# Kernel optimization log

Measured on AMD Instinct MI355X. Metric: run time of the kernel, lower is better.

The kernel has to match this reference:

```python
import jax, jax.numpy as jnp
import numpy as np
from jax import lax

B, S, N, FD = 4, 12, 307, 3
E = 64; F = 64; H = 64; K = 3; HEADS = 4; P = 12; DFF = 64


def setup_inputs() -> dict:
    key = jax.random.key(0)
    ks = jax.random.split(key, 24)
    rn = lambda i, shape, s=0.1: jax.random.normal(ks[i], shape, dtype=jnp.float32) * s
    z = lambda n: jnp.zeros((n,), jnp.float32)
    return {
        'x': jax.random.normal(ks[0], (B, S, N, FD), dtype=jnp.float32),
        'cheb': rn(1, (K, N, N), 0.05),
        'theta': rn(2, (K, E, F)),
        'W_emb_x': rn(3, (1, E)), 'b_emb_x': z(E),
        'W_emb_os': rn(4, (FD - 1, E)), 'b_emb_os': z(E),
        'U_x': rn(5, (F, 4 * H)), 'V_x': rn(6, (H, 4 * H)), 'b_x': z(4 * H),
        'U_g': rn(7, (F, 2 * H)), 'V_g': rn(8, (H, 2 * H)), 'b_g': z(2 * H),
        'W_ff1': rn(9, (H, DFF)), 'b_ff1': z(DFF), 'W_ff2': rn(10, (DFF, H)), 'b_ff2': z(H),
        'W_tc': rn(11, (F, H, 1, 3)), 'b_tc': z(F),
        'W_rc': rn(12, (F, H, 1, 1)), 'b_rc': z(F),
        'W_in': rn(13, (3 * F, F)), 'b_in': z(3 * F),
        'W_out': rn(14, (F, F)), 'b_out': z(F),
        'W_fa1': rn(15, (F, DFF)), 'b_fa1': z(DFF), 'W_fa2': rn(16, (DFF, F)), 'b_fa2': z(F),
        'W_fin': rn(17, (P, S, 1, F)), 'b_fin': z(P),
    }


def _forward(x, cheb, theta, W_emb_x, b_emb_x, W_emb_os, b_emb_os,
             U_x, V_x, b_x, U_g, V_g, b_g, W_ff1, b_ff1, W_ff2, b_ff2,
             W_tc, b_tc, W_rc, b_rc, W_in, b_in, W_out, b_out,
             W_fa1, b_fa1, W_fa2, b_fa2, W_fin, b_fin):
    # token embeddings (dropout=0 -> identity)
    emb_x = x[..., :1] @ W_emb_x + b_emb_x          # (B,S,N,E)
    emb_os = x[..., 1:] @ W_emb_os + b_emb_os       # (B,S,N,E)

    def cheb_conv(h):
        # sum_k relu-after-sum of T_k @ h @ theta_k
        agg = jnp.einsum('kmn,bsnc->kbsmc', cheb, h)
        return jax.nn.relu(jnp.einsum('kbsmc,kcd->bsmd', agg, theta))

    gcn_x = cheb_conv(emb_x)                        # (B,S,N,F)
    gcn_os = cheb_conv(emb_os)                      # (B,S,N,F)

    # Glstm: precompute input projections, scan the recurrence over time
    gx = jnp.einsum('bsnc,cf->sbnf', gcn_x, U_x) + b_x    # (S,B,N,4H)
    gg = jnp.einsum('bsnc,cf->sbnf', gcn_os, U_g) + b_g   # (S,B,N,2H)

    h0 = jnp.zeros((B, N, H), x.dtype)
    c0 = jnp.zeros((B, N, H), x.dtype)

    def step(carry, inp):
        ht, ct = carry
        gx_t, gg_t = inp
        gates = jax.nn.sigmoid(gx_t + ht @ V_x)     # ft,it,ot,ut all sigmoid (as in source)
        gov = jax.nn.sigmoid(gg_t + ht @ V_g)
        ft, it, ot, ut = jnp.split(gates, 4, axis=-1)
        gf, gu = jnp.split(gov, 2, axis=-1)
        ct = gf * ft * ct + gu * it * ut
        ht = ot * jnp.tanh(ct)
        return (ht, ct), ht

    _, hs = lax.scan(step, (h0, c0), (gx, gg))
    hidden = jnp.moveaxis(hs, 0, 1)                 # (B,S,N,H)
    # Muti_glstm output feedforward
    hidden = jax.nn.relu(hidden @ W_ff1 + b_ff1) @ W_ff2 + b_ff2

    # time conv: (1,3) kernel over time axis, pad 1
    hs_nchw = jnp.transpose(hidden, (0, 3, 2, 1))   # (B,H,N,S)
    tc = lax.conv_general_dilated(hs_nchw, W_tc, (1, 1), ((0, 0), (1, 1)),
                                  dimension_numbers=('NCHW', 'OIHW', 'NCHW'))
    tc = jnp.transpose(tc + b_tc[None, :, None, None], (0, 3, 2, 1))  # (B,S,N,F)

    # query = last time step, repeated over S
    query = jnp.broadcast_to(tc[:, -1:], (B, S, N, F))
    q_in = jnp.reshape(jnp.swapaxes(query, 2, 3), (B * N, S, F))
    kv_in = jnp.reshape(jnp.swapaxes(emb_x, 2, 3), (B * N, S, E))

    # torch MHA (batch_first=False): seq axis is dim0 (L=B*N), batch axis is dim1 (S)
    hd = F // HEADS
    Wq, Wk, Wv = jnp.split(W_in, 3, axis=0)
    bq, bk, bv = jnp.split(b_in, 3)

    def proj(t, Wp, bp):
        L = t.shape[0]
        p = t @ Wp.T + bp                            # (L, S, F)
        return jnp.transpose(p.reshape(L, S * HEADS, hd), (1, 0, 2))  # (S*HEADS, L, hd)

    qh = proj(q_in, Wq, bq)
    kh = proj(kv_in, Wk, bk)
    vh = proj(kv_in, Wv, bv)
    scores = jnp.einsum('hld,hmd->hlm', qh, kh) / np.float32(np.sqrt(hd))
    attn = jax.nn.softmax(scores, axis=-1)
    ctx = jnp.einsum('hlm,hmd->hld', attn, vh)       # (S*HEADS, B*N, hd)
    ctx = jnp.transpose(ctx, (1, 0, 2)).reshape(B * N, S, F)
    dsa = ctx @ W_out.T + b_out                      # (B*N, S, F)

    dsa = jnp.swapaxes(dsa.reshape(B, N, S, F), 1, 2)  # (B,S,N,F)
    ffa = jax.nn.relu(dsa @ W_fa1 + b_fa1) @ W_fa2 + b_fa2
    # residual 1x1 conv over channels of hidden
    res = jnp.einsum('bsnh,fh->bsnf', hidden, W_rc[:, :, 0, 0]) + b_rc
    comb = res + ffa                                 # (B,S,N,F)
    # final conv: channels=S, kernel (1,F) valid, then take last width index
    out = jnp.einsum('bsnf,psf->bpn', comb, W_fin[:, :, 0, :]) + b_fin[None, :, None]
    return out                                       # (B, pre_len, N)


def reference(x, cheb, theta, W_emb_x, b_emb_x, W_emb_os, b_emb_os,
              U_x, V_x, b_x, U_g, V_g, b_g, W_ff1, b_ff1, W_ff2, b_ff2,
              W_tc, b_tc, W_rc, b_rc, W_in, b_in, W_out, b_out,
              W_fa1, b_fa1, W_fa2, b_fa2, W_fin, b_fin):
    return _forward(x, cheb, theta, W_emb_x, b_emb_x, W_emb_os, b_emb_os,
                    U_x, V_x, b_x, U_g, V_g, b_g, W_ff1, b_ff1, W_ff2, b_ff2,
                    W_tc, b_tc, W_rc, b_rc, W_in, b_in, W_out, b_out,
                    W_fa1, b_fa1, W_fa2, b_fa2, W_fin, b_fin)
```

## Files before the change

kernel.cpp:

```cpp
#include <hip/hip_runtime.h>
#include <hip/hip_bf16.h>

#define BB 4
#define SS 12
#define NN 307
#define LL 1228
#define BSC 48
#define GG 48
#define WS_CX    0
#define WS_CROW  132624
#define WS_TXD   133568
#define WS_TBD   133760
#define WS_T1D   133952
#define WS_T2D   134144
#define WS_TOB   134336
#define WS_WRCT  134528
#define WS_WOT   138624
#define WS_H2    142720
#define WS_TFL   1085824
#define WS_XFL   1164416
#define WS_QH    2107520
#define WS_KH    3050624
#define WS_VH    3993728
#define WS_CTX   4936832

__global__ __launch_bounds__(256) void k1_precomp(
    const float* __restrict__ theta, const float* __restrict__ Wex,
    const float* __restrict__ bex, const float* __restrict__ Weos,
    const float* __restrict__ beos, const float* __restrict__ W_rc,
    const float* __restrict__ W_out, float* __restrict__ ws) {
  int tid = threadIdx.x;
  if (tid < 192) {
    int k = tid / 64, d = tid % 64;
    float a0 = 0.f, a1 = 0.f, a2 = 0.f, a3 = 0.f, a4 = 0.f;
    for (int c = 0; c < 64; ++c) {
      float th = theta[(k * 64 + c) * 64 + d];
      a0 = fmaf(Wex[c], th, a0);
      a1 = fmaf(bex[c], th, a1);
      a2 = fmaf(Weos[c], th, a2);
      a3 = fmaf(Weos[64 + c], th, a3);
      a4 = fmaf(beos[c], th, a4);
    }
    ws[WS_TXD + tid] = a0; ws[WS_TBD + tid] = a1; ws[WS_T1D + tid] = a2;
    ws[WS_T2D + tid] = a3; ws[WS_TOB + tid] = a4;
  }
  for (int i = tid; i < 4096; i += 256) {
    int hh = i >> 6, f = i & 63;
    ws[WS_WRCT + i] = W_rc[f * 64 + hh];
    ws[WS_WOT + i]  = W_out[f * 64 + hh];
  }
}

__global__ __launch_bounds__(320) void k2_cx(const float* __restrict__ x,
                                             const float* __restrict__ cheb,
                                             float* __restrict__ ws) {
  int k = blockIdx.x / BSC, bs = blockIdx.x % BSC;
  __shared__ float xl[921];
  for (int i = threadIdx.x; i < 921; i += 320) xl[i] = x[bs * 921 + i];
  __syncthreads();
  int m = threadIdx.x;
  if (m < NN) {
    const float* ch = cheb + (k * NN + m) * NN;
    float a0 = 0.f, a1 = 0.f, a2 = 0.f, ar = 0.f;
    for (int n = 0; n < NN; ++n) {
      float c = ch[n];
      ar += c;
      a0 = fmaf(c, xl[3 * n], a0);
      a1 = fmaf(c, xl[3 * n + 1], a1);
      a2 = fmaf(c, xl[3 * n + 2], a2);
    }
    ws[WS_CX + ((k * 3 + 0) * BSC + bs) * NN + m] = a0;
    ws[WS_CX + ((k * 3 + 1) * BSC + bs) * NN + m] = a1;
    ws[WS_CX + ((k * 3 + 2) * BSC + bs) * NN + m] = a2;
    if (bs == 0) ws[WS_CROW + k * NN + m] = ar;
  }
}

__global__ __launch_bounds__(256) void k2c_xfl(const float* __restrict__ x,
                                               const float* __restrict__ Wex,
                                               const float* __restrict__ bex,
                                               float* __restrict__ ws) {
  int idx = blockIdx.x * 256 + threadIdx.x;
  if (idx < 943104) {
    int n = idx % NN;
    int t = idx / NN;
    int e = t & 63;
    int bs = t >> 6;
    ws[WS_XFL + idx] = fmaf(x[(bs * NN + n) * 3], Wex[e], bex[e]);
  }
}

__global__ __launch_bounds__(384) void k3_scan(
    const float* __restrict__ U_x, const float* __restrict__ V_x,
    const float* __restrict__ b_x, const float* __restrict__ U_g,
    const float* __restrict__ V_g, const float* __restrict__ b_g,
    const float* __restrict__ W_ff1, const float* __restrict__ b_ff1,
    const float* __restrict__ W_ff2, const float* __restrict__ b_ff2,
    const float* __restrict__ W_tc, const float* __restrict__ b_tc,
    float* __restrict__ ws) {
  int l = blockIdx.x;
  int b = l / NN, n = l % NN;
  int tid = threadIdx.x;
  __shared__ float gcx[768], gcos[768], hsb[768], sg[256], sv[128];

  for (int idx = tid; idx < 768; idx += 384) {
    int s = idx >> 6, d = idx & 63;
    int bs = b * SS + s;
    float ax = 0.f, ao = 0.f;
#pragma unroll
    for (int k = 0; k < 3; ++k) {
      float c0 = ws[WS_CX + ((k * 3 + 0) * BSC + bs) * NN + n];
      float c1 = ws[WS_CX + ((k * 3 + 1) * BSC + bs) * NN + n];
      float c2 = ws[WS_CX + ((k * 3 + 2) * BSC + bs) * NN + n];
      float cr = ws[WS_CROW + k * NN + n];
      ax += c0 * ws[WS_TXD + k * 64 + d] + cr * ws[WS_TBD + k * 64 + d];
      ao += c1 * ws[WS_T1D + k * 64 + d] + c2 * ws[WS_T2D + k * 64 + d] +
            cr * ws[WS_TOB + k * 64 + d];
    }
    gcx[idx] = fmaxf(ax, 0.f);
    gcos[idx] = fmaxf(ao, 0.f);
  }
  __syncthreads();

  float gr[12];
  float vcol[64];
  if (tid < 256) {
#pragma unroll
    for (int s = 0; s < 12; ++s) gr[s] = b_x[tid];
    for (int c4 = 0; c4 < 16; ++c4) {
      float u0 = U_x[(4 * c4 + 0) * 256 + tid];
      float u1 = U_x[(4 * c4 + 1) * 256 + tid];
      float u2 = U_x[(4 * c4 + 2) * 256 + tid];
      float u3 = U_x[(4 * c4 + 3) * 256 + tid];
#pragma unroll
      for (int s = 0; s < 12; ++s) {
        float4 g = *reinterpret_cast<const float4*>(&gcx[s * 64 + 4 * c4]);
        gr[s] = fmaf(g.x, u0, fmaf(g.y, u1, fmaf(g.z, u2, fmaf(g.w, u3, gr[s]))));
      }
    }
#pragma unroll
    for (int c = 0; c < 64; ++c) vcol[c] = V_x[c * 256 + tid];
  } else {
    int j = tid - 256;
#pragma unroll
    for (int s = 0; s < 12; ++s) gr[s] = b_g[j];
    for (int c4 = 0; c4 < 16; ++c4) {
      float u0 = U_g[(4 * c4 + 0) * 128 + j];
      float u1 = U_g[(4 * c4 + 1) * 128 + j];
      float u2 = U_g[(4 * c4 + 2) * 128 + j];
      float u3 = U_g[(4 * c4 + 3) * 128 + j];
#pragma unroll
      for (int s = 0; s < 12; ++s) {
        float4 g = *reinterpret_cast<const float4*>(&gcos[s * 64 + 4 * c4]);
        gr[s] = fmaf(g.x, u0, fmaf(g.y, u1, fmaf(g.z, u2, fmaf(g.w, u3, gr[s]))));
      }
    }
#pragma unroll
    for (int c = 0; c < 64; ++c) vcol[c] = V_g[c * 128 + j];
  }

  float ct = 0.f;
  for (int s = 0; s < 12; ++s) {
    float a = gr[s];
    if (s > 0) {
      const float* hp = &hsb[(s - 1) * 64];
      float a0 = 0.f, a1 = 0.f, a2 = 0.f, a3 = 0.f;
#pragma unroll
      for (int c4 = 0; c4 < 16; c4 += 4) {
        float4 h0 = *reinterpret_cast<const float4*>(&hp[4 * c4]);
        float4 h1 = *reinterpret_cast<const float4*>(&hp[4 * c4 + 4]);
        float4 h2 = *reinterpret_cast<const float4*>(&hp[4 * c4 + 8]);
        float4 h3 = *reinterpret_cast<const float4*>(&hp[4 * c4 + 12]);
        a0 = fmaf(h0.x, vcol[4 * c4 + 0], fmaf(h0.y, vcol[4 * c4 + 1],
             fmaf(h0.z, vcol[4 * c4 + 2], fmaf(h0.w, vcol[4 * c4 + 3], a0))));
        a1 = fmaf(h1.x, vcol[4 * c4 + 4], fmaf(h1.y, vcol[4 * c4 + 5],
             fmaf(h1.z, vcol[4 * c4 + 6], fmaf(h1.w, vcol[4 * c4 + 7], a1))));
        a2 = fmaf(h2.x, vcol[4 * c4 + 8], fmaf(h2.y, vcol[4 * c4 + 9],
             fmaf(h2.z, vcol[4 * c4 + 10], fmaf(h2.w, vcol[4 * c4 + 11], a2))));
        a3 = fmaf(h3.x, vcol[4 * c4 + 12], fmaf(h3.y, vcol[4 * c4 + 13],
             fmaf(h3.z, vcol[4 * c4 + 14], fmaf(h3.w, vcol[4 * c4 + 15], a3))));
      }
      a += (a0 + a1) + (a2 + a3);
    }
    float sig = 1.f / (1.f + __expf(-a));
    if (tid < 256) sg[tid] = sig; else sv[tid - 256] = sig;
    __syncthreads();
    if (tid < 64) {
      ct = sv[tid] * sg[tid] * ct + sv[64 + tid] * sg[64 + tid] * sg[192 + tid];
      hsb[s * 64 + tid] = sg[128 + tid] * tanhf(ct);
    }
    __syncthreads();
  }

  for (int idx = tid; idx < 768; idx += 384) {
    int s = idx >> 6, d = idx & 63;
    float acc = b_ff1[d];
    for (int c4 = 0; c4 < 16; ++c4) {
      float4 h4 = *reinterpret_cast<const float4*>(&hsb[s * 64 + 4 * c4]);
      acc = fmaf(h4.x, W_ff1[(4 * c4 + 0) * 64 + d],
            fmaf(h4.y, W_ff1[(4 * c4 + 1) * 64 + d],
            fmaf(h4.z, W_ff1[(4 * c4 + 2) * 64 + d],
            fmaf(h4.w, W_ff1[(4 * c4 + 3) * 64 + d], acc))));
    }
    gcx[idx] = fmaxf(acc, 0.f);
  }
  __syncthreads();
  for (int idx = tid; idx < 768; idx += 384) {
    int s = idx >> 6, h = idx & 63;
    float acc = b_ff2[h];
    for (int c4 = 0; c4 < 16; ++c4) {
      float4 t4 = *reinterpret_cast<const float4*>(&gcx[s * 64 + 4 * c4]);
      acc = fmaf(t4.x, W_ff2[(4 * c4 + 0) * 64 + h],
            fmaf(t4.y, W_ff2[(4 * c4 + 1) * 64 + h],
            fmaf(t4.z, W_ff2[(4 * c4 + 2) * 64 + h],
            fmaf(t4.w, W_ff2[(4 * c4 + 3) * 64 + h], acc))));
    }
    ws[WS_H2 + ((b * SS + s) * NN + n) * 64 + h] = acc;
    gcos[idx] = acc;
  }
  __syncthreads();
  if (tid < 64) {
    int f = tid;
    float acc = b_tc[f];
    for (int h = 0; h < 64; ++h) {
      acc = fmaf(gcos[10 * 64 + h], W_tc[(f * 64 + h) * 3 + 0], acc);
      acc = fmaf(gcos[11 * 64 + h], W_tc[(f * 64 + h) * 3 + 1], acc);
    }
    ws[WS_TFL + (b * 64 + f) * NN + n] = acc;
  }
}

__global__ __launch_bounds__(256) void k5_qkv(const float* __restrict__ W_in,
                                              const float* __restrict__ b_in,
                                              float* __restrict__ ws) {
  int blk = blockIdx.x;
  int g = blk / 77, mt = blk % 77;
  int s = g >> 2, a = g & 3;
  int m0 = mt * 16;
  __shared__ float xw[16][64], qw[16][64];
  for (int i = threadIdx.x; i < 1024; i += 256) {
    int mi = i >> 6, e = i & 63;
    int m = m0 + mi;
    if (m < LL) {
      int base = m * 768 + s * 64;
      xw[mi][e] = ws[WS_XFL + base + e];
      int bq = base / 235776;
      int off = base % 19648;
      qw[mi][e] = ws[WS_TFL + bq * 19648 + off + e];
    }
  }
  __syncthreads();
  int mi = threadIdx.x >> 4, d = threadIdx.x & 15;
  int m = m0 + mi;
  if (m < LL) {
    int f = a * 16 + d;
    float aq = b_in[f], ak = b_in[64 + f], av = b_in[128 + f];
    for (int e = 0; e < 64; ++e) {
      aq = fmaf(qw[mi][e], W_in[f * 64 + e], aq);
      ak = fmaf(xw[mi][e], W_in[(64 + f) * 64 + e], ak);
      av = fmaf(xw[mi][e], W_in[(128 + f) * 64 + e], av);
    }
    int o = (g * LL + m) * 16 + d;
    ws[WS_QH + o] = aq; ws[WS_KH + o] = ak; ws[WS_VH + o] = av;
  }
}

__global__ __launch_bounds__(512) void k6_attn(float* __restrict__ ws) {
  int blk = blockIdx.x;
  int g = blk / 10, qt = blk % 10;
  int s = g >> 2, a = g & 3;
  int tid = threadIdx.x;
  int w = tid >> 6;
  int qi = tid & 63;
  int l0 = qt * 128 + qi;
  int l1 = l0 + 64;
  bool act0 = (l0 < LL), act1 = (l1 < LL);

  __shared__ float sh[9728];
  float4* kt4 = reinterpret_cast<float4*>(sh);
  float4* vt4 = reinterpret_cast<float4*>(sh + 4096);

  float q0[16], q1[16], cx0[16], cx1[16];
  if (act0) {
    const float4* qp = reinterpret_cast<const float4*>(ws + WS_QH + (g * LL + l0) * 16);
#pragma unroll
    for (int jj = 0; jj < 4; ++jj) {
      float4 t = qp[jj];
      q0[4 * jj] = t.x * 0.25f; q0[4 * jj + 1] = t.y * 0.25f;
      q0[4 * jj + 2] = t.z * 0.25f; q0[4 * jj + 3] = t.w * 0.25f;
    }
  } else {
#pragma unroll
    for (int d = 0; d < 16; ++d) q0[d] = 0.f;
  }
  if (act1) {
    const float4* qp = reinterpret_cast<const float4*>(ws + WS_QH + (g * LL + l1) * 16);
#pragma unroll
    for (int jj = 0; jj < 4; ++jj) {
      float4 t = qp[jj];
      q1[4 * jj] = t.x * 0.25f; q1[4 * jj + 1] = t.y * 0.25f;
      q1[4 * jj + 2] = t.z * 0.25f; q1[4 * jj + 3] = t.w * 0.25f;
    }
  } else {
#pragma unroll
    for (int d = 0; d < 16; ++d) q1[d] = 0.f;
  }
#pragma unroll
  for (int d = 0; d < 16; ++d) { cx0[d] = 0.f; cx1[d] = 0.f; }
  float den0 = 0.f, den1 = 0.f;

  const float4* kb = reinterpret_cast<const float4*>(ws + WS_KH + g * LL * 16);
  const float4* vb = reinterpret_cast<const float4*>(ws + WS_VH + g * LL * 16);

  for (int mt = 0; mt < 5; ++mt) {
    int mbase = mt * 256;
    int cnt = LL - mbase; if (cnt > 256) cnt = 256;
    int nf4 = cnt * 4;
    for (int i = tid; i < nf4; i += 512) {
      kt4[i] = kb[mbase * 4 + i];
      vt4[i] = vb[mbase * 4 + i];
    }
    __syncthreads();
    int e0 = w * 32;
    int e1 = e0 + 32; if (e1 > cnt) e1 = cnt;
    for (int mi = e0; mi < e1; ++mi) {
      float4 ka = kt4[mi * 4], kbb = kt4[mi * 4 + 1];
      float4 kc = kt4[mi * 4 + 2], kd = kt4[mi * 4 + 3];
      float p0 = q0[0] * ka.x, p1 = q1[0] * ka.x;
      p0 = fmaf(q0[1], ka.y, p0);   p1 = fmaf(q1[1], ka.y, p1);
      p0 = fmaf(q0[2], ka.z, p0);   p1 = fmaf(q1[2], ka.z, p1);
      p0 = fmaf(q0[3], ka.w, p0);   p1 = fmaf(q1[3], ka.w, p1);
      p0 = fmaf(q0[4], kbb.x, p0);  p1 = fmaf(q1[4], kbb.x, p1);
      p0 = fmaf(q0[5], kbb.y, p0);  p1 = fmaf(q1[5], kbb.y, p1);
      p0 = fmaf(q0[6], kbb.z, p0);  p1 = fmaf(q1[6], kbb.z, p1);
      p0 = fmaf(q0[7], kbb.w, p0);  p1 = fmaf(q1[7], kbb.w, p1);
      p0 = fmaf(q0[8], kc.x, p0);   p1 = fmaf(q1[8], kc.x, p1);
      p0 = fmaf(q0[9], kc.y, p0);   p1 = fmaf(q1[9], kc.y, p1);
      p0 = fmaf(q0[10], kc.z, p0);  p1 = fmaf(q1[10], kc.z, p1);
      p0 = fmaf(q0[11], kc.w, p0);  p1 = fmaf(q1[11], kc.w, p1);
      p0 = fmaf(q0[12], kd.x, p0);  p1 = fmaf(q1[12], kd.x, p1);
      p0 = fmaf(q0[13], kd.y, p0);  p1 = fmaf(q1[13], kd.y, p1);
      p0 = fmaf(q0[14], kd.z, p0);  p1 = fmaf(q1[14], kd.z, p1);
      p0 = fmaf(q0[15], kd.w, p0);  p1 = fmaf(q1[15], kd.w, p1);
      float e0w = __expf(fminf(p0, 60.f));
      float e1w = __expf(fminf(p1, 60.f));
      den0 += e0w; den1 += e1w;
      float4 va = vt4[mi * 4], vbb = vt4[mi * 4 + 1];
      float4 vc = vt4[mi * 4 + 2], vd = vt4[mi * 4 + 3];
      cx0[0]  = fmaf(e0w, va.x, cx0[0]);   cx1[0]  = fmaf(e1w, va.x, cx1[0]);
      cx0[1]  = fmaf(e0w, va.y, cx0[1]);   cx1[1]  = fmaf(e1w, va.y, cx1[1]);
      cx0[2]  = fmaf(e0w, va.z, cx0[2]);   cx1[2]  = fmaf(e1w, va.z, cx1[2]);
      cx0[3]  = fmaf(e0w, va.w, cx0[3]);   cx1[3]  = fmaf(e1w, va.w, cx1[3]);
      cx0[4]  = fmaf(e0w, vbb.x, cx0[4]);  cx1[4]  = fmaf(e1w, vbb.x, cx1[4]);
      cx0[5]  = fmaf(e0w, vbb.y, cx0[5]);  cx1[5]  = fmaf(e1w, vbb.y, cx1[5]);
      cx0[6]  = fmaf(e0w, vbb.z, cx0[6]);  cx1[6]  = fmaf(e1w, vbb.z, cx1[6]);
      cx0[7]  = fmaf(e0w, vbb.w, cx0[7]);  cx1[7]  = fmaf(e1w, vbb.w, cx1[7]);
      cx0[8]  = fmaf(e0w, vc.x, cx0[8]);   cx1[8]  = fmaf(e1w, vc.x, cx1[8]);
      cx0[9]  = fmaf(e0w, vc.y, cx0[9]);   cx1[9]  = fmaf(e1w, vc.y, cx1[9]);
      cx0[10] = fmaf(e0w, vc.z, cx0[10]);  cx1[10] = fmaf(e1w, vc.z, cx1[10]);
      cx0[11] = fmaf(e0w, vc.w, cx0[11]);  cx1[11] = fmaf(e1w, vc.w, cx1[11]);
      cx0[12] = fmaf(e0w, vd.x, cx0[12]);  cx1[12] = fmaf(e1w, vd.x, cx1[12]);
      cx0[13] = fmaf(e0w, vd.y, cx0[13]);  cx1[13] = fmaf(e1w, vd.y, cx1[13]);
      cx0[14] = fmaf(e0w, vd.z, cx0[14]);  cx1[14] = fmaf(e1w, vd.z, cx1[14]);
      cx0[15] = fmaf(e0w, vd.w, cx0[15]);  cx1[15] = fmaf(e1w, vd.w, cx1[15]);
    }
    __syncthreads();
  }

  float* sden = sh;
  float* scx  = sh + 512;
#pragma unroll
  for (int ph = 0; ph < 2; ++ph) {
    sden[w * 64 + qi] = ph ? den1 : den0;
    const float* cxp = ph ? cx1 : cx0;
#pragma unroll
    for (int d = 0; d < 16; ++d) scx[(w * 64 + qi) * 17 + d] = cxp[d];
    __syncthreads();
    if (tid < 256) {
      int q2 = tid >> 2, jj = tid & 3;
      int l2 = qt * 128 + ph * 64 + q2;
      if (l2 < LL) {
        float dtot = 0.f, c0 = 0.f, c1 = 0.f, c2 = 0.f, c3 = 0.f;
#pragma unroll
        for (int u = 0; u < 8; ++u) {
          dtot += sden[u * 64 + q2];
          const float* cp = &scx[(u * 64 + q2) * 17 + jj * 4];
          c0 += cp[0]; c1 += cp[1]; c2 += cp[2]; c3 += cp[3];
        }
        float inv = 1.f / dtot;
        float* op = ws + WS_CTX + (l2 * SS + s) * 64 + a * 16 + jj * 4;
        *reinterpret_cast<float4*>(op) =
            make_float4(c0 * inv, c1 * inv, c2 * inv, c3 * inv);
      }
    }
    __syncthreads();
  }
}

__global__ __launch_bounds__(64) void k7a_comb(
    const float* __restrict__ W_fa1, const float* __restrict__ b_fa1,
    const float* __restrict__ W_fa2, const float* __restrict__ b_fa2,
    const float* __restrict__ b_rc, const float* __restrict__ b_out,
    float* __restrict__ ws) {
  int blk = blockIdx.x;
  int l = blk / SS, s = blk % SS;
  int b = l / NN, n = l % NN;
  int f = threadIdx.x;
  __shared__ float h2r[64], ctr[64], dsrL[64], trL[64];

  h2r[f] = ws[WS_H2 + ((b * SS + s) * NN + n) * 64 + f];
  ctr[f] = ws[WS_CTX + (l * SS + s) * 64 + f];
  __syncthreads();

  float dsr = b_out[f], res = b_rc[f];
  for (int q = 0; q < 64; ++q) {
    dsr = fmaf(ctr[q], ws[WS_WOT + q * 64 + f], dsr);
    res = fmaf(h2r[q], ws[WS_WRCT + q * 64 + f], res);
  }
  dsrL[f] = dsr;
  __syncthreads();

  float t = b_fa1[f];
  for (int q = 0; q < 64; ++q) t = fmaf(dsrL[q], W_fa1[q * 64 + f], t);
  trL[f] = fmaxf(t, 0.f);
  __syncthreads();

  float ff = b_fa2[f];
  for (int q = 0; q < 64; ++q) ff = fmaf(trL[q], W_fa2[q * 64 + f], ff);
  ws[WS_XFL + (l * SS + s) * 64 + f] = res + ff;
}

__global__ __launch_bounds__(320) void k7b_fin(
    const float* __restrict__ W_fin, const float* __restrict__ b_fin,
    const float* __restrict__ ws, float* __restrict__ out) {
  int blk = blockIdx.x;
  int b = blk / SS, p = blk % SS;
  int tid = threadIdx.x;
  __shared__ float wf[768];
  for (int i = tid; i < 768; i += 320) wf[i] = W_fin[p * 768 + i];
  __syncthreads();
  int n = tid;
  if (n < NN) {
    const float* cb = ws + WS_XFL + (b * NN + n) * 768;
    float a0 = 0.f, a1 = 0.f, a2 = 0.f, a3 = 0.f;
    for (int i = 0; i < 768; i += 4) {
      a0 = fmaf(cb[i], wf[i], a0);
      a1 = fmaf(cb[i + 1], wf[i + 1], a1);
      a2 = fmaf(cb[i + 2], wf[i + 2], a2);
      a3 = fmaf(cb[i + 3], wf[i + 3], a3);
    }
    out[(b * SS + p) * NN + n] = (a0 + a1) + (a2 + a3) + b_fin[p];
  }
}

extern "C" void kernel_launch(void* const* d_in, const int* in_sizes, int n_in,
                              void* d_out, int out_size, void* d_ws, size_t ws_size,
                              hipStream_t stream) {
  (void)in_sizes; (void)n_in; (void)out_size; (void)ws_size;
  const float* x     = (const float*)d_in[0];
  const float* cheb  = (const float*)d_in[1];
  const float* theta = (const float*)d_in[2];
  const float* Wex   = (const float*)d_in[3];
  const float* bex   = (const float*)d_in[4];
  const float* Weos  = (const float*)d_in[5];
  const float* beos  = (const float*)d_in[6];
  const float* U_x   = (const float*)d_in[7];
  const float* V_x   = (const float*)d_in[8];
  const float* b_x   = (const float*)d_in[9];
  const float* U_g   = (const float*)d_in[10];
  const float* V_g   = (const float*)d_in[11];
  const float* b_g   = (const float*)d_in[12];
  const float* W_ff1 = (const float*)d_in[13];
  const float* b_ff1 = (const float*)d_in[14];
  const float* W_ff2 = (const float*)d_in[15];
  const float* b_ff2 = (const float*)d_in[16];
  const float* W_tc  = (const float*)d_in[17];
  const float* b_tc  = (const float*)d_in[18];
  const float* W_rc  = (const float*)d_in[19];
  const float* b_rc  = (const float*)d_in[20];
  const float* W_in  = (const float*)d_in[21];
  const float* b_in  = (const float*)d_in[22];
  const float* W_out = (const float*)d_in[23];
  const float* b_out = (const float*)d_in[24];
  const float* W_fa1 = (const float*)d_in[25];
  const float* b_fa1 = (const float*)d_in[26];
  const float* W_fa2 = (const float*)d_in[27];
  const float* b_fa2 = (const float*)d_in[28];
  const float* W_fin = (const float*)d_in[29];
  const float* b_fin = (const float*)d_in[30];
  float* ws = (float*)d_ws;
  float* outp = (float*)d_out;

  k1_precomp<<<1, 256, 0, stream>>>(theta, Wex, bex, Weos, beos, W_rc, W_out, ws);
  k2_cx<<<144, 320, 0, stream>>>(x, cheb, ws);
  k2c_xfl<<<3684, 256, 0, stream>>>(x, Wex, bex, ws);
  k3_scan<<<1228, 384, 0, stream>>>(U_x, V_x, b_x, U_g, V_g, b_g,
                                    W_ff1, b_ff1, W_ff2, b_ff2, W_tc, b_tc, ws);
  k5_qkv<<<48 * 77, 256, 0, stream>>>(W_in, b_in, ws);
  k6_attn<<<480, 512, 0, stream>>>(ws);
  k7a_comb<<<LL * SS, 64, 0, stream>>>(W_fa1, b_fa1, W_fa2, b_fa2,
                                       b_rc, b_out, ws);
  k7b_fin<<<BB * SS, 320, 0, stream>>>(W_fin, b_fin, ws, outp);
}
```

Before: 366.1 us.

## Fuse prep kernels and use wave shuffles in LSTM scan to drop a barrier

Merges the three preprocessing kernels into a single launch with block-index dispatch, cutting launch overhead. In the recurrent scan, every wave now redundantly computes the cell state and broadcasts h via wave shuffles instead of LDS. The gate buffers are double-buffered so only one __syncthreads per step is needed. This trades redundant tanh/ALU work and shuffle traffic for fewer barriers and less LDS use.

```diff
diff --git a/kernel.cpp b/kernel.cpp
--- a/kernel.cpp
+++ b/kernel.cpp
@@ -24,69 +24,64 @@
 #define WS_VH    3993728
 #define WS_CTX   4936832
 
-__global__ __launch_bounds__(256) void k1_precomp(
+__global__ __launch_bounds__(320) void k12_fused(
+    const float* __restrict__ x, const float* __restrict__ cheb,
     const float* __restrict__ theta, const float* __restrict__ Wex,
     const float* __restrict__ bex, const float* __restrict__ Weos,
     const float* __restrict__ beos, const float* __restrict__ W_rc,
     const float* __restrict__ W_out, float* __restrict__ ws) {
+  int blk = blockIdx.x;
   int tid = threadIdx.x;
-  if (tid < 192) {
-    int k = tid / 64, d = tid % 64;
-    float a0 = 0.f, a1 = 0.f, a2 = 0.f, a3 = 0.f, a4 = 0.f;
-    for (int c = 0; c < 64; ++c) {
-      float th = theta[(k * 64 + c) * 64 + d];
-      a0 = fmaf(Wex[c], th, a0);
-      a1 = fmaf(bex[c], th, a1);
-      a2 = fmaf(Weos[c], th, a2);
-      a3 = fmaf(Weos[64 + c], th, a3);
-      a4 = fmaf(beos[c], th, a4);
-    }
-    ws[WS_TXD + tid] = a0; ws[WS_TBD + tid] = a1; ws[WS_T1D + tid] = a2;
-    ws[WS_T2D + tid] = a3; ws[WS_TOB + tid] = a4;
-  }
-  for (int i = tid; i < 4096; i += 256) {
-    int hh = i >> 6, f = i & 63;
-    ws[WS_WRCT + i] = W_rc[f * 64 + hh];
-    ws[WS_WOT + i]  = W_out[f * 64 + hh];
-  }
-}
-
-__global__ __launch_bounds__(320) void k2_cx(const float* __restrict__ x,
-                                             const float* __restrict__ cheb,
-                                             float* __restrict__ ws) {
-  int k = blockIdx.x / BSC, bs = blockIdx.x % BSC;
-  __shared__ float xl[921];
-  for (int i = threadIdx.x; i < 921; i += 320) xl[i] = x[bs * 921 + i];
-  __syncthreads();
-  int m = threadIdx.x;
-  if (m < NN) {
-    const float* ch = cheb + (k * NN + m) * NN;
-    float a0 = 0.f, a1 = 0.f, a2 = 0.f, ar = 0.f;
-    for (int n = 0; n < NN; ++n) {
-      float c = ch[n];
-      ar += c;
-      a0 = fmaf(c, xl[3 * n], a0);
-      a1 = fmaf(c, xl[3 * n + 1], a1);
-      a2 = fmaf(c, xl[3 * n + 2], a2);
-    }
-    ws[WS_CX + ((k * 3 + 0) * BSC + bs) * NN + m] = a0;
-    ws[WS_CX + ((k * 3 + 1) * BSC + bs) * NN + m] = a1;
-    ws[WS_CX + ((k * 3 + 2) * BSC + bs) * NN + m] = a2;
-    if (bs == 0) ws[WS_CROW + k * NN + m] = ar;
-  }
-}
-
-__global__ __launch_bounds__(256) void k2c_xfl(const float* __restrict__ x,
-                                               const float* __restrict__ Wex,
-                                               const float* __restrict__ bex,
-                                               float* __restrict__ ws) {
-  int idx = blockIdx.x * 256 + threadIdx.x;
-  if (idx < 943104) {
-    int n = idx % NN;
-    int t = idx / NN;
-    int e = t & 63;
-    int bs = t >> 6;
-    ws[WS_XFL + idx] = fmaf(x[(bs * NN + n) * 3], Wex[e], bex[e]);
+  if (blk < 144) {
+    int k = blk / BSC, bs = blk % BSC;
+    __shared__ float xl[921];
+    for (int i = tid; i < 921; i += 320) xl[i] = x[bs * 921 + i];
+    __syncthreads();
+    int m = tid;
+    if (m < NN) {
+      const float* ch = cheb + (k * NN + m) * NN;
+      float a0 = 0.f, a1 = 0.f, a2 = 0.f, ar = 0.f;
+      for (int n = 0; n < NN; ++n) {
+        float c = ch[n];
+        ar += c;
+        a0 = fmaf(c, xl[3 * n], a0);
+        a1 = fmaf(c, xl[3 * n + 1], a1);
+        a2 = fmaf(c, xl[3 * n + 2], a2);
+      }
+      ws[WS_CX + ((k * 3 + 0) * BSC + bs) * NN + m] = a0;
+      ws[WS_CX + ((k * 3 + 1) * BSC + bs) * NN + m] = a1;
+      ws[WS_CX + ((k * 3 + 2) * BSC + bs) * NN + m] = a2;
+      if (bs == 0) ws[WS_CROW + k * NN + m] = ar;
+    }
+  } else if (blk < 3092) {
+    int idx = (blk - 144) * 320 + tid;
+    if (idx < 943104) {
+      int n = idx % NN;
+      int t = idx / NN;
+      int e = t & 63;
+      int bs = t >> 6;
+      ws[WS_XFL + idx] = fmaf(x[(bs * NN + n) * 3], Wex[e], bex[e]);
+    }
+  } else {
+    if (tid < 192) {
+      int k = tid / 64, d = tid % 64;
+      float a0 = 0.f, a1 = 0.f, a2 = 0.f, a3 = 0.f, a4 = 0.f;
+      for (int c = 0; c < 64; ++c) {
+        float th = theta[(k * 64 + c) * 64 + d];
+        a0 = fmaf(Wex[c], th, a0);
+        a1 = fmaf(bex[c], th, a1);
+        a2 = fmaf(Weos[c], th, a2);
+        a3 = fmaf(Weos[64 + c], th, a3);
+        a4 = fmaf(beos[c], th, a4);
+      }
+      ws[WS_TXD + tid] = a0; ws[WS_TBD + tid] = a1; ws[WS_T1D + tid] = a2;
+      ws[WS_T2D + tid] = a3; ws[WS_TOB + tid] = a4;
+    }
+    for (int i = tid; i < 4096; i += 320) {
+      int hh = i >> 6, f = i & 63;
+      ws[WS_WRCT + i] = W_rc[f * 64 + hh];
+      ws[WS_WOT + i]  = W_out[f * 64 + hh];
+    }
   }
 }
 
@@ -101,7 +96,7 @@
   int l = blockIdx.x;
   int b = l / NN, n = l % NN;
   int tid = threadIdx.x;
-  __shared__ float gcx[768], gcos[768], hsb[768], sg[256], sv[128];
+  __shared__ float gcx[768], gcos[768], hsb[768], sg[512], sv[256];
 
   for (int idx = tid; idx < 768; idx += 384) {
     int s = idx >> 6, d = idx & 63;
@@ -141,14 +136,14 @@
 #pragma unroll
     for (int c = 0; c < 64; ++c) vcol[c] = V_x[c * 256 + tid];
   } else {
-    int j = tid - 256;
-#pragma unroll
-    for (int s = 0; s < 12; ++s) gr[s] = b_g[j];
+    int j2 = tid - 256;
+#pragma unroll
+    for (int s = 0; s < 12; ++s) gr[s] = b_g[j2];
     for (int c4 = 0; c4 < 16; ++c4) {
-      float u0 = U_g[(4 * c4 + 0) * 128 + j];
-      float u1 = U_g[(4 * c4 + 1) * 128 + j];
-      float u2 = U_g[(4 * c4 + 2) * 128 + j];
-      float u3 = U_g[(4 * c4 + 3) * 128 + j];
+      float u0 = U_g[(4 * c4 + 0) * 128 + j2];
+      float u1 = U_g[(4 * c4 + 1) * 128 + j2];
+      float u2 = U_g[(4 * c4 + 2) * 128 + j2];
+      float u3 = U_g[(4 * c4 + 3) * 128 + j2];
 #pragma unroll
       for (int s = 0; s < 12; ++s) {
         float4 g = *reinterpret_cast<const float4*>(&gcos[s * 64 + 4 * c4]);
@@ -156,41 +151,37 @@
       }
     }
 #pragma unroll
-    for (int c = 0; c < 64; ++c) vcol[c] = V_g[c * 128 + j];
-  }
-
-  float ct = 0.f;
+    for (int c = 0; c < 64; ++c) vcol[c] = V_g[c * 128 + j2];
+  }
+
+  int j = tid & 63;
+  float ct = 0.f, h = 0.f;
   for (int s = 0; s < 12; ++s) {
     float a = gr[s];
     if (s > 0) {
-      const float* hp = &hsb[(s - 1) * 64];
       float a0 = 0.f, a1 = 0.f, a2 = 0.f, a3 = 0.f;
 #pragma unroll
-      for (int c4 = 0; c4 < 16; c4 += 4) {
-        float4 h0 = *reinterpret_cast<const float4*>(&hp[4 * c4]);
-        float4 h1 = *reinterpret_cast<const float4*>(&hp[4 * c4 + 4]);
-        float4 h2 = *reinterpret_cast<const float4*>(&hp[4 * c4 + 8]);
-        float4 h3 = *reinterpret_cast<const float4*>(&hp[4 * c4 + 12]);
-        a0 = fmaf(h0.x, vcol[4 * c4 + 0], fmaf(h0.y, vcol[4 * c4 + 1],
-             fmaf(h0.z, vcol[4 * c4 + 2], fmaf(h0.w, vcol[4 * c4 + 3], a0))));
-        a1 = fmaf(h1.x, vcol[4 * c4 + 4], fmaf(h1.y, vcol[4 * c4 + 5],
-             fmaf(h1.z, vcol[4 * c4 + 6], fmaf(h1.w, vcol[4 * c4 + 7], a1))));
-        a2 = fmaf(h2.x, vcol[4 * c4 + 8], fmaf(h2.y, vcol[4 * c4 + 9],
-             fmaf(h2.z, vcol[4 * c4 + 10], fmaf(h2.w, vcol[4 * c4 + 11], a2))));
-        a3 = fmaf(h3.x, vcol[4 * c4 + 12], fmaf(h3.y, vcol[4 * c4 + 13],
-             fmaf(h3.z, vcol[4 * c4 + 14], fmaf(h3.w, vcol[4 * c4 + 15], a3))));
+      for (int c = 0; c < 64; c += 4) {
+        a0 = fmaf(__shfl(h, c + 0, 64), vcol[c + 0], a0);
+        a1 = fmaf(__shfl(h, c + 1, 64), vcol[c + 1], a1);
+        a2 = fmaf(__shfl(h, c + 2, 64), vcol[c + 2], a2);
+        a3 = fmaf(__shfl(h, c + 3, 64), vcol[c + 3], a3);
       }
       a += (a0 + a1) + (a2 + a3);
     }
     float sig = 1.f / (1.f + __expf(-a));
-    if (tid < 256) sg[tid] = sig; else sv[tid - 256] = sig;
-    __syncthreads();
-    if (tid < 64) {
-      ct = sv[tid] * sg[tid] * ct + sv[64 + tid] * sg[64 + tid] * sg[192 + tid];
-      hsb[s * 64 + tid] = sg[128 + tid] * tanhf(ct);
-    }
-    __syncthreads();
-  }
+    int p = s & 1;
+    if (tid < 256) sg[p * 256 + tid] = sig;
+    else sv[p * 128 + (tid - 256)] = sig;
+    __syncthreads();
+    float ft = sg[p * 256 + j],       it = sg[p * 256 + 64 + j];
+    float ot = sg[p * 256 + 128 + j], ut = sg[p * 256 + 192 + j];
+    float gf = sv[p * 128 + j],       gu = sv[p * 128 + 64 + j];
+    ct = gf * ft * ct + gu * it * ut;
+    h = ot * tanhf(ct);
+    if (tid < 64) hsb[s * 64 + j] = h;
+  }
+  __syncthreads();
 
   for (int idx = tid; idx < 768; idx += 384) {
     int s = idx >> 6, d = idx & 63;
@@ -206,25 +197,25 @@
   }
   __syncthreads();
   for (int idx = tid; idx < 768; idx += 384) {
-    int s = idx >> 6, h = idx & 63;
-    float acc = b_ff2[h];
+    int s = idx >> 6, hh = idx & 63;
+    float acc = b_ff2[hh];
     for (int c4 = 0; c4 < 16; ++c4) {
       float4 t4 = *reinterpret_cast<const float4*>(&gcx[s * 64 + 4 * c4]);
-      acc = fmaf(t4.x, W_ff2[(4 * c4 + 0) * 64 + h],
-            fmaf(t4.y, W_ff2[(4 * c4 + 1) * 64 + h],
-            fmaf(t4.z, W_ff2[(4 * c4 + 2) * 64 + h],
-            fmaf(t4.w, W_ff2[(4 * c4 + 3) * 64 + h], acc))));
-    }
-    ws[WS_H2 + ((b * SS + s) * NN + n) * 64 + h] = acc;
+      acc = fmaf(t4.x, W_ff2[(4 * c4 + 0) * 64 + hh],
+            fmaf(t4.y, W_ff2[(4 * c4 + 1) * 64 + hh],
+            fmaf(t4.z, W_ff2[(4 * c4 + 2) * 64 + hh],
+            fmaf(t4.w, W_ff2[(4 * c4 + 3) * 64 + hh], acc))));
+    }
+    ws[WS_H2 + ((b * SS + s) * NN + n) * 64 + hh] = acc;
     gcos[idx] = acc;
   }
   __syncthreads();
   if (tid < 64) {
     int f = tid;
     float acc = b_tc[f];
-    for (int h = 0; h < 64; ++h) {
-      acc = fmaf(gcos[10 * 64 + h], W_tc[(f * 64 + h) * 3 + 0], acc);
-      acc = fmaf(gcos[11 * 64 + h], W_tc[(f * 64 + h) * 3 + 1], acc);
+    for (int hh = 0; hh < 64; ++hh) {
+      acc = fmaf(gcos[10 * 64 + hh], W_tc[(f * 64 + hh) * 3 + 0], acc);
+      acc = fmaf(gcos[11 * 64 + hh], W_tc[(f * 64 + hh) * 3 + 1], acc);
     }
     ws[WS_TFL + (b * 64 + f) * NN + n] = acc;
   }
@@ -491,9 +482,8 @@
   float* ws = (float*)d_ws;
   float* outp = (float*)d_out;
 
-  k1_precomp<<<1, 256, 0, stream>>>(theta, Wex, bex, Weos, beos, W_rc, W_out, ws);
-  k2_cx<<<144, 320, 0, stream>>>(x, cheb, ws);
-  k2c_xfl<<<3684, 256, 0, stream>>>(x, Wex, bex, ws);
+  k12_fused<<<3093, 320, 0, stream>>>(x, cheb, theta, Wex, bex, Weos, beos,
+                                      W_rc, W_out, ws);
   k3_scan<<<1228, 384, 0, stream>>>(U_x, V_x, b_x, U_g, V_g, b_g,
                                     W_ff1, b_ff1, W_ff2, b_ff2, W_tc, b_tc, ws);
   k5_qkv<<<48 * 77, 256, 0, stream>>>(W_in, b_in, ws);
```

After: 394.9 us. 1.08x slower.
